# Optimization experiments

Hardware: AMD Instinct MI355X
Metric: run time of the kernel (lower is better)

Reference implementation:

```python
import jax, jax.numpy as jnp
import numpy as np
from jax.scipy.stats import norm

K = 2               # select_experts
NOISE_EPS = 0.01
LOSS_COEF = 0.01
CV_EPS = 1e-10


def setup_inputs() -> dict:
    key = jax.random.key(0)
    ks = jax.random.split(key, 8)
    N, D, H, E = 8192, 1024, 4096, 8
    s_in = 1.0 / np.sqrt(D)
    s_h = 1.0 / np.sqrt(H)
    return {
        "x": jax.random.normal(ks[0], (N, D), jnp.float32),
        "noise": jax.random.normal(ks[1], (N, E), jnp.float32),
        "w_gate": jax.random.normal(ks[2], (D, E), jnp.float32) * s_in,
        "w_noise": jax.random.normal(ks[3], (D, E), jnp.float32) * s_in,
        "W1": jax.random.normal(ks[4], (E, D, H), jnp.float32) * s_in,
        "b1": jnp.zeros((E, H), jnp.float32),
        "W2": jax.random.normal(ks[5], (E, H, D), jnp.float32) * s_h,
        "b2": jnp.zeros((E, D), jnp.float32),
    }


def _cv_squared(v):
    # torch .var() is unbiased (ddof=1)
    return v.var(ddof=1) / (v.mean() ** 2 + CV_EPS)


def reference(x, noise, w_gate, w_noise, W1, b1, W2, b2):
    N = x.shape[0]
    # --- noisy top-k gating (training path) ---
    clean_logits = x @ w_gate                                  # [N, E]
    noise_stddev = jax.nn.softplus(x @ w_noise) + NOISE_EPS    # [N, E]
    noisy_logits = clean_logits + noise * noise_stddev         # [N, E]
    top_vals, top_idx = jax.lax.top_k(noisy_logits, K + 1)     # [N, K+1]
    top_k_gates = jax.nn.softmax(top_vals[:, :K], axis=1)      # [N, K]
    gates = jnp.zeros_like(noisy_logits).at[
        jnp.arange(N)[:, None], top_idx[:, :K]
    ].set(top_k_gates)                                         # [N, E]

    # --- load (prob of being in top-k under the gating noise) ---
    thr_in = top_vals[:, K:K + 1]                              # [N, 1]
    thr_out = top_vals[:, K - 1:K]                             # [N, 1]
    is_in = noisy_logits > thr_in
    prob_in = norm.cdf((clean_logits - thr_in) / noise_stddev)
    prob_out = norm.cdf((clean_logits - thr_out) / noise_stddev)
    load = jnp.where(is_in, prob_in, prob_out).sum(0)          # [E]

    importance = gates.sum(0)                                  # [E]
    loss = (_cv_squared(importance) + _cv_squared(load)) * LOSS_COEF

    # --- dense all-expert stack, masked by sparse gates ---
    h = jax.nn.relu(jnp.einsum('nd,edh->neh', x, W1) + b1)     # [N, E, H]
    out = jnp.einsum('neh,ehd->ned', h, W2) + b2               # [N, E, D]
    y = jnp.einsum('ned,ne->nd', out, gates)                   # [N, D]
    return y, loss
```

## Files before the change

### kernel.cpp

```cpp
#include <hip/hip_runtime.h>

typedef unsigned short u16;
typedef unsigned int u32;
typedef __attribute__((ext_vector_type(4))) float f32x4;
typedef __attribute__((ext_vector_type(8))) short short8;
typedef __attribute__((ext_vector_type(4))) unsigned short u16x4;

#define BARR __builtin_amdgcn_s_barrier()
#define VM4  asm volatile("s_waitcnt vmcnt(4)" ::: "memory")
#define VM0  asm volatile("s_waitcnt vmcnt(0)" ::: "memory")

__device__ __forceinline__ u16 f2b(float f){
  u32 u = __float_as_uint(f);
  u = (u + 0x7FFFu + ((u >> 16) & 1u)) >> 16;
  return (u16)u;
}
__device__ __forceinline__ float b2f(u16 h){ return __uint_as_float(((u32)h) << 16); }

__device__ __forceinline__ void gload16(const void* g, void* l){
  __builtin_amdgcn_global_load_lds((__attribute__((address_space(1))) void*)(g),
                                   (__attribute__((address_space(3))) void*)(l), 16, 0, 0);
}

__global__ __launch_bounds__(256) void transpose_cvt_kernel(const float* __restrict__ src,
                                                            u16* __restrict__ dst,
                                                            int R, int C){
  __shared__ float t[64][65];
  int e = blockIdx.z;
  size_t eo = (size_t)R * C * e;
  int c0 = blockIdx.x * 64, r0 = blockIdx.y * 64;
  int tid = threadIdx.x;
  int lr = tid >> 4, lc4 = (tid & 15) * 4;
  #pragma unroll
  for (int i = 0; i < 4; i++){
    int r = lr + i * 16;
    float4 v = *(const float4*)&src[eo + (size_t)(r0 + r) * C + c0 + lc4];
    t[r][lc4] = v.x; t[r][lc4 + 1] = v.y; t[r][lc4 + 2] = v.z; t[r][lc4 + 3] = v.w;
  }
  __syncthreads();
  #pragma unroll
  for (int i = 0; i < 4; i++){
    int c = lr + i * 16;
    u16x4 o = { f2b(t[lc4][c]), f2b(t[lc4 + 1][c]), f2b(t[lc4 + 2][c]), f2b(t[lc4 + 3][c]) };
    *(u16x4*)&dst[eo + (size_t)(c0 + c) * R + r0 + lc4] = o;
  }
}

__global__ __launch_bounds__(256) void gating_kernel(const float* __restrict__ x,
                                                     const float* __restrict__ nz,
                                                     const float* __restrict__ wg,
                                                     const float* __restrict__ wn,
                                                     int* __restrict__ counts,
                                                     int4* __restrict__ rowinfo,
                                                     float* __restrict__ loadrow,
                                                     u16* __restrict__ xb){
  __shared__ float wpart[16][4][17];
  int tid = threadIdx.x, w = tid >> 6, lane = tid & 63;
  int d0 = w * 256 + lane * 4;
  float4 wgA[4], wgB[4], wnA[4], wnB[4];
  #pragma unroll
  for (int k = 0; k < 4; k++){
    wgA[k] = *(const float4*)&wg[(d0 + k) * 8];
    wgB[k] = *(const float4*)&wg[(d0 + k) * 8 + 4];
    wnA[k] = *(const float4*)&wn[(d0 + k) * 8];
    wnB[k] = *(const float4*)&wn[(d0 + k) * 8 + 4];
  }
  int rbase = blockIdx.x * 16;
  for (int r = 0; r < 16; r++){
    int row = rbase + r;
    float4 xv = *(const float4*)&x[(size_t)row * 1024 + d0];
    u16x4 xo = { f2b(xv.x), f2b(xv.y), f2b(xv.z), f2b(xv.w) };
    *(u16x4*)&xb[(size_t)row * 1024 + d0] = xo;
    float ag[8], an[8];
    #pragma unroll
    for (int e = 0; e < 8; e++){ ag[e] = 0.f; an[e] = 0.f; }
    float xk[4] = { xv.x, xv.y, xv.z, xv.w };
    #pragma unroll
    for (int k = 0; k < 4; k++){
      ag[0] = fmaf(xk[k], wgA[k].x, ag[0]); ag[1] = fmaf(xk[k], wgA[k].y, ag[1]);
      ag[2] = fmaf(xk[k], wgA[k].z, ag[2]); ag[3] = fmaf(xk[k], wgA[k].w, ag[3]);
      ag[4] = fmaf(xk[k], wgB[k].x, ag[4]); ag[5] = fmaf(xk[k], wgB[k].y, ag[5]);
      ag[6] = fmaf(xk[k], wgB[k].z, ag[6]); ag[7] = fmaf(xk[k], wgB[k].w, ag[7]);
      an[0] = fmaf(xk[k], wnA[k].x, an[0]); an[1] = fmaf(xk[k], wnA[k].y, an[1]);
      an[2] = fmaf(xk[k], wnA[k].z, an[2]); an[3] = fmaf(xk[k], wnA[k].w, an[3]);
      an[4] = fmaf(xk[k], wnB[k].x, an[4]); an[5] = fmaf(xk[k], wnB[k].y, an[5]);
      an[6] = fmaf(xk[k], wnB[k].z, an[6]); an[7] = fmaf(xk[k], wnB[k].w, an[7]);
    }
    #pragma unroll
    for (int off = 32; off >= 1; off >>= 1){
      #pragma unroll
      for (int e = 0; e < 8; e++){
        ag[e] += __shfl_xor(ag[e], off, 64);
        an[e] += __shfl_xor(an[e], off, 64);
      }
    }
    if (lane == 0){
      #pragma unroll
      for (int e = 0; e < 8; e++){
        wpart[r][w][e] = ag[e];
        wpart[r][w][8 + e] = an[e];
      }
    }
  }
  __syncthreads();
  if (tid < 16){
    int r = tid, row = rbase + r;
    float cg[16];
    #pragma unroll
    for (int v = 0; v < 16; v++)
      cg[v] = wpart[r][0][v] + wpart[r][1][v] + wpart[r][2][v] + wpart[r][3][v];
    float clean[8], sd[8], noisy[8];
    #pragma unroll
    for (int e = 0; e < 8; e++){
      clean[e] = cg[e];
      float v = cg[8 + e];
      float sp = fmaxf(v, 0.f) + log1pf(expf(-fabsf(v)));
      sd[e] = sp + 0.01f;
      noisy[e] = clean[e] + nz[row * 8 + e] * sd[e];
    }
    int i0 = 0, i1 = -1;
    float b0 = -3.4e38f, b1v = -3.4e38f, b2v = -3.4e38f;
    #pragma unroll
    for (int j = 0; j < 8; j++){
      float t = noisy[j];
      if (t > b0){ b2v = b1v; b1v = b0; i1 = i0; b0 = t; i0 = j; }
      else if (t > b1v){ b2v = b1v; b1v = t; i1 = j; }
      else if (t > b2v){ b2v = t; }
    }
    float eg = expf(b1v - b0);
    float g0 = 1.f / (1.f + eg), g1 = eg / (1.f + eg);
    rowinfo[row] = make_int4(i0, i1, __float_as_int(g0), __float_as_int(g1));
    atomicAdd(&counts[i0], 1);
    atomicAdd(&counts[i1], 1);
    float thr_in = b2v, thr_out = b1v;
    #pragma unroll
    for (int e = 0; e < 8; e++){
      bool isin = noisy[e] > thr_in;
      float thr = isin ? thr_in : thr_out;
      float z = (clean[e] - thr) / sd[e];
      loadrow[row * 8 + e] = 0.5f * (1.f + erff(z * 0.70710678118654752f));
    }
  }
}

__global__ void scan_kernel(const int* __restrict__ counts, int* __restrict__ offs,
                            int* __restrict__ btab){
  if (threadIdx.x == 0){
    int s = 0, nb = 0;
    for (int e = 0; e < 8; e++){
      offs[e] = s;
      int c = counts[e]; s += c;
      int nbe = (c + 255) >> 8;
      for (int t = 0; t < nbe; t++) btab[nb++] = (e << 16) | t;
    }
    offs[15] = nb;
  }
}

__global__ __launch_bounds__(256) void fill_kernel(const int4* __restrict__ rowinfo,
                                                   const int* __restrict__ offs,
                                                   int* __restrict__ cnt2,
                                                   int* __restrict__ tok,
                                                   int* __restrict__ slot_of){
  int r = blockIdx.x * 256 + threadIdx.x;
  int4 ri = rowinfo[r];
  int p0 = atomicAdd(&cnt2[ri.x], 1);
  int s0 = offs[ri.x] + p0;
  tok[s0] = r; slot_of[2 * r] = s0;
  int p1 = atomicAdd(&cnt2[ri.y], 1);
  int s1 = offs[ri.y] + p1;
  tok[s1] = r; slot_of[2 * r + 1] = s1;
}

template<int KDIM, bool GATHER, bool RELU, bool PSPLIT>
__global__ __launch_bounds__(512, 1) void ffn8_kernel(
    const u16* __restrict__ Ag, const u16* __restrict__ Bt,
    const float* __restrict__ bias, u16* __restrict__ outp,
    const int* __restrict__ counts, const int* __restrict__ offs,
    const int* __restrict__ btab, const int* __restrict__ tok,
    int nc, int klen, int ostr, size_t pstride)
{
  __shared__ u16 As[2][2][128 * 64];
  __shared__ u16 Bs[2][2][128 * 64];

  int gx = gridDim.x;
  int lin = blockIdx.y * gx + blockIdx.x;
  int total = gx * gridDim.y, chunk = total >> 3;
  int swz = (lin & 7) * chunk + (lin >> 3);
  int bx = swz % gx, tq = swz / gx;
  int nblk = offs[15];
  if (bx >= nblk) return;
  int kh = tq / nc;
  int tn = tq - kh * nc;
  int kbase = kh * klen;
  int niter = klen >> 7;
  int et = btab[bx]; int e = et >> 16, tm = et & 0xffff;
  int cnt = counts[e], off_e = offs[e];

  int tid = threadIdx.x, lane = tid & 63;
  int wid = tid >> 6, wm = wid >> 2, wn = wid & 3;

  int rl0 = tid >> 3, c8 = tid & 7;
  const char* Abase = (const char*)Ag + (size_t)kbase * 2;
  const char* Bbase = (const char*)(Bt + (size_t)e * 4194304) + (size_t)kbase * 2;
  u32 aoff[4], boff[4];
  #pragma unroll
  for (int h = 0; h < 2; h++)
    #pragma unroll
    for (int r = 0; r < 2; r++){
      int rl = h * 128 + r * 64 + rl0;
      int c8s = c8 ^ (rl & 7);
      int rr = tm * 256 + rl;
      int rc = (rr < cnt) ? rr : (cnt - 1);
      size_t arow = GATHER ? (size_t)tok[off_e + rc] : (size_t)(off_e + rc);
      aoff[h * 2 + r] = (u32)(arow * (KDIM * 2) + c8s * 16);
      boff[h * 2 + r] = (u32)((size_t)(tn * 256 + rl) * (KDIM * 2) + c8s * 16);
    }
  int ldst = (tid & ~63) * 8;

  auto stA = [&](int b, int h, int t){
    const char* s = Abase + (size_t)t * 128;
    gload16(s + aoff[h * 2 + 0], &As[b][h][ldst]);
    gload16(s + aoff[h * 2 + 1], &As[b][h][4096 + ldst]);
  };
  auto stB = [&](int b, int h, int t){
    const char* s = Bbase + (size_t)t * 128;
    gload16(s + boff[h * 2 + 0], &Bs[b][h][ldst]);
    gload16(s + boff[h * 2 + 1], &Bs[b][h][4096 + ldst]);
  };

  int lm = lane & 15, lkb = (lane >> 4) * 8;
  short8 Ar[4][2], Br[2][2][2];
  auto ldA = [&](int b, int rh){
    #pragma unroll
    for (int ii = 0; ii < 4; ii++){
      int rl = rh * 64 + ii * 16 + lm;
      #pragma unroll
      for (int ks = 0; ks < 2; ks++){
        int idx = (rl * 64 + ks * 32 + lkb) ^ ((rl & 7) << 3);
        Ar[ii][ks] = *(const short8*)&As[b][wm][idx];
      }
    }
  };
  auto ldB = [&](int b, int ch){
    #pragma unroll
    for (int jj = 0; jj < 2; jj++){
      int rb = wn * 64 + ch * 32 + jj * 16 + lm;
      int hB = rb >> 7, rl = rb & 127;
      #pragma unroll
      for (int ks = 0; ks < 2; ks++){
        int idx = (rl * 64 + ks * 32 + lkb) ^ ((rl & 7) << 3);
        Br[ch][jj][ks] = *(const short8*)&Bs[b][hB][idx];
      }
    }
  };

  f32x4 acc[8][4];
  #pragma unroll
  for (int i = 0; i < 8; i++)
    #pragma unroll
    for (int j = 0; j < 4; j++) acc[i][j] = (f32x4){0.f, 0.f, 0.f, 0.f};

  auto mfmaQ = [&](int rh, int ch){
    __builtin_amdgcn_s_setprio(1);
    #pragma unroll
    for (int ks = 0; ks < 2; ks++)
      #pragma unroll
      for (int ii = 0; ii < 4; ii++)
        #pragma unroll
        for (int jj = 0; jj < 2; jj++)
          acc[rh * 4 + ii][ch * 2 + jj] = __builtin_amdgcn_mfma_f32_16x16x32_bf16(
              Ar[ii][ks], Br[ch][jj][ks], acc[rh * 4 + ii][ch * 2 + jj], 0, 0, 0);
    __builtin_amdgcn_s_setprio(0);
  };

  stA(0, 0, 0); stA(0, 1, 0); stB(0, 0, 0); stB(0, 1, 0);
  stB(1, 0, 1); stA(1, 0, 1);
  VM4; BARR;

  for (int j = 0; j < niter - 1; ++j){
    int t1 = 2 * j + 1, t2 = 2 * j + 2, t3 = 2 * j + 3;
    ldA(0, 0); ldB(0, 0);
    stA(1, 1, t1);
    BARR; mfmaQ(0, 0); ldB(0, 1); BARR;
    stB(1, 1, t1);
    BARR; mfmaQ(0, 1); ldA(0, 1); BARR;
    stB(0, 0, t2);
    BARR; mfmaQ(1, 1); BARR;
    stA(0, 0, t2);
    BARR; mfmaQ(1, 0); VM4; BARR;
    ldA(1, 0); ldB(1, 0);
    stA(0, 1, t2);
    BARR; mfmaQ(0, 0); ldB(1, 1); BARR;
    stB(0, 1, t2);
    BARR; mfmaQ(0, 1); ldA(1, 1); BARR;
    stB(1, 0, t3);
    BARR; mfmaQ(1, 1); BARR;
    stA(1, 0, t3);
    BARR; mfmaQ(1, 0); VM4; BARR;
  }

  {
    int t1 = (klen >> 6) - 1;
    ldA(0, 0); ldB(0, 0);
    stA(1, 1, t1);
    BARR; mfmaQ(0, 0); ldB(0, 1); BARR;
    stB(1, 1, t1);
    BARR; mfmaQ(0, 1); ldA(0, 1); BARR;
    BARR; mfmaQ(1, 1); BARR;
    mfmaQ(1, 0); VM0; BARR;
    ldA(1, 0); ldB(1, 0);
    BARR; mfmaQ(0, 0); ldB(1, 1); BARR;
    BARR; mfmaQ(0, 1); ldA(1, 1); BARR;
    BARR; mfmaQ(1, 1); BARR;
    mfmaQ(1, 0);
  }

  int lr = (lane >> 4) * 4;
  u16* po = outp + (PSPLIT ? (size_t)kh * pstride : 0);
  #pragma unroll
  for (int i = 0; i < 8; i++){
    int row_l = wm * 128 + i * 16 + lr;
    #pragma unroll
    for (int jj = 0; jj < 4; jj++){
      int col = tn * 256 + wn * 64 + jj * 16 + lm;
      float bv = PSPLIT ? 0.f : bias[e * ostr + col];
      #pragma unroll
      for (int q = 0; q < 4; q++){
        int r = tm * 256 + row_l + q;
        if (r < cnt){
          float v = acc[i][jj][q] + bv;
          if (RELU) v = fmaxf(v, 0.f);
          po[(size_t)(off_e + r) * ostr + col] = f2b(v);
        }
      }
    }
  }
}

__global__ __launch_bounds__(256) void combine_kernel(const u16* __restrict__ pb,
                                                      const float* __restrict__ b2,
                                                      const int4* __restrict__ rowinfo,
                                                      const int* __restrict__ slot_of,
                                                      float* __restrict__ y){
  const size_t PS = (size_t)16384 * 1024;
  int g = blockIdx.x * 256 + threadIdx.x;
  int row = g >> 8;
  int c4 = (g & 255) * 4;
  int4 ri = rowinfo[row];
  float g0 = __int_as_float(ri.z), g1 = __int_as_float(ri.w);
  int s0 = slot_of[2 * row], s1 = slot_of[2 * row + 1];
  float4 sum0 = *(const float4*)&b2[(ri.x << 10) + c4];
  float4 sum1 = *(const float4*)&b2[(ri.y << 10) + c4];
  #pragma unroll
  for (int kh = 0; kh < 4; kh++){
    u16x4 a = *(const u16x4*)&pb[kh * PS + ((size_t)s0 << 10) + c4];
    u16x4 b = *(const u16x4*)&pb[kh * PS + ((size_t)s1 << 10) + c4];
    sum0.x += b2f(a.x); sum0.y += b2f(a.y); sum0.z += b2f(a.z); sum0.w += b2f(a.w);
    sum1.x += b2f(b.x); sum1.y += b2f(b.y); sum1.z += b2f(b.z); sum1.w += b2f(b.w);
  }
  float4 o;
  o.x = g0 * sum0.x + g1 * sum1.x;
  o.y = g0 * sum0.y + g1 * sum1.y;
  o.z = g0 * sum0.z + g1 * sum1.z;
  o.w = g0 * sum0.w + g1 * sum1.w;
  *(float4*)&y[(size_t)row * 1024 + c4] = o;
}

__global__ __launch_bounds__(256) void loss1_kernel(const int4* __restrict__ rowinfo,
                                                    const float* __restrict__ loadrow,
                                                    float* __restrict__ partials){
  __shared__ float part[16][256];
  int tid = threadIdx.x;
  int r = blockIdx.x * 256 + tid;
  int4 ri = rowinfo[r];
  float g0 = __int_as_float(ri.z), g1 = __int_as_float(ri.w);
  f32x4 l0 = *(const f32x4*)&loadrow[r * 8];
  f32x4 l1 = *(const f32x4*)&loadrow[r * 8 + 4];
  #pragma unroll
  for (int e = 0; e < 8; e++){
    part[e][tid] = ((ri.x == e) ? g0 : 0.f) + ((ri.y == e) ? g1 : 0.f);
    part[8 + e][tid] = (e < 4) ? l0[e & 3] : l1[e & 3];
  }
  __syncthreads();
  #pragma unroll
  for (int s = 128; s >= 1; s >>= 1){
    if (tid < s){
      #pragma unroll
      for (int e = 0; e < 16; e++) part[e][tid] += part[e][tid + s];
    }
    __syncthreads();
  }
  if (tid < 16) partials[blockIdx.x * 16 + tid] = part[tid][0];
}

__global__ __launch_bounds__(64) void loss2_kernel(const float* __restrict__ partials,
                                                   float* __restrict__ out_loss){
  __shared__ float tot[16];
  int tid = threadIdx.x;
  if (tid < 16){
    float s = 0.f;
    for (int b = 0; b < 32; b++) s += partials[b * 16 + tid];
    tot[tid] = s;
  }
  __syncthreads();
  if (tid == 0){
    float mi = 0.f, ml = 0.f;
    for (int e = 0; e < 8; e++){ mi += tot[e]; ml += tot[8 + e]; }
    mi *= 0.125f; ml *= 0.125f;
    float vi = 0.f, vl = 0.f;
    for (int e = 0; e < 8; e++){
      float di = tot[e] - mi; vi += di * di;
      float dl = tot[8 + e] - ml; vl += dl * dl;
    }
    vi /= 7.f; vl /= 7.f;
    float cvi = vi / (mi * mi + 1e-10f);
    float cvl = vl / (ml * ml + 1e-10f);
    out_loss[0] = 0.01f * (cvi + cvl);
  }
}

extern "C" void kernel_launch(void* const* d_in, const int* in_sizes, int n_in,
                              void* d_out, int out_size, void* d_ws, size_t ws_size,
                              hipStream_t stream){
  const float* x  = (const float*)d_in[0];
  const float* nz = (const float*)d_in[1];
  const float* wg = (const float*)d_in[2];
  const float* wn = (const float*)d_in[3];
  const float* W1 = (const float*)d_in[4];
  const float* b1 = (const float*)d_in[5];
  const float* W2 = (const float*)d_in[6];
  const float* b2 = (const float*)d_in[7];
  float* y = (float*)d_out;
  float* loss = y + (size_t)8192 * 1024;

  char* ws = (char*)d_ws;
  size_t o = 0;
  auto alloc = [&](size_t bytes){ size_t r = o; o += (bytes + 255) & ~(size_t)255; return r; };
  int*  counts  = (int*)(ws + alloc(64));
  int*  cnt2    = (int*)(ws + alloc(64));
  int*  offs    = (int*)(ws + alloc(64));
  int*  btab    = (int*)(ws + alloc(1024));
  int4* rowinfo = (int4*)(ws + alloc((size_t)8192 * 16));
  int*  slot_of = (int*)(ws + alloc((size_t)16384 * 4));
  int*  tok     = (int*)(ws + alloc((size_t)16384 * 4));
  float* loadrow = (float*)(ws + alloc((size_t)8192 * 8 * 4));
  float* partials = (float*)(ws + alloc(32 * 16 * 4));
  u16*  xb      = (u16*)(ws + alloc((size_t)8192 * 1024 * 2));
  u16*  w1t     = (u16*)(ws + alloc((size_t)8 * 1024 * 4096 * 2));
  u16*  w2t     = (u16*)(ws + alloc((size_t)8 * 1024 * 4096 * 2));
  u16*  h_buf   = (u16*)(ws + alloc((size_t)16384 * 4096 * 2));
  u16*  pbuf    = (u16*)(ws + alloc((size_t)4 * 16384 * 1024 * 2));
  if (o > ws_size) return;

  hipMemsetAsync(ws, 0, 768, stream);

  gating_kernel<<<512, 256, 0, stream>>>(x, nz, wg, wn, counts, rowinfo, loadrow, xb);
  transpose_cvt_kernel<<<dim3(64, 16, 8), 256, 0, stream>>>(W1, w1t, 1024, 4096);
  transpose_cvt_kernel<<<dim3(16, 64, 8), 256, 0, stream>>>(W2, w2t, 4096, 1024);
  scan_kernel<<<1, 64, 0, stream>>>(counts, offs, btab);
  fill_kernel<<<32, 256, 0, stream>>>(rowinfo, offs, cnt2, tok, slot_of);
  ffn8_kernel<1024, true, true, false><<<dim3(72, 16), 512, 0, stream>>>(
      xb, w1t, b1, h_buf, counts, offs, btab, tok, 16, 1024, 4096, 0);
  ffn8_kernel<4096, false, false, true><<<dim3(72, 16), 512, 0, stream>>>(
      h_buf, w2t, nullptr, pbuf, counts, offs, btab, tok, 4, 1024, 1024,
      (size_t)16384 * 1024);
  combine_kernel<<<8192, 256, 0, stream>>>(pbuf, b2, rowinfo, slot_of, y);
  loss1_kernel<<<32, 256, 0, stream>>>(rowinfo, loadrow, partials);
  loss2_kernel<<<1, 64, 0, stream>>>(partials, loss);
}
```

Before: 685.4 us.

## Stage GEMM epilogue through LDS for coalesced stores, merge scan into fill

Result: slower. 710.0 us (+3.6%).

```diff
diff --git a/kernel.cpp b/kernel.cpp
--- a/kernel.cpp
+++ b/kernel.cpp
@@ -143,32 +143,35 @@
   }
 }
 
-__global__ void scan_kernel(const int* __restrict__ counts, int* __restrict__ offs,
-                            int* __restrict__ btab){
-  if (threadIdx.x == 0){
-    int s = 0, nb = 0;
-    for (int e = 0; e < 8; e++){
-      offs[e] = s;
-      int c = counts[e]; s += c;
-      int nbe = (c + 255) >> 8;
-      for (int t = 0; t < nbe; t++) btab[nb++] = (e << 16) | t;
-    }
-    offs[15] = nb;
-  }
-}
-
-__global__ __launch_bounds__(256) void fill_kernel(const int4* __restrict__ rowinfo,
-                                                   const int* __restrict__ offs,
+__global__ __launch_bounds__(256) void fill_kernel(const int* __restrict__ counts,
+                                                   const int4* __restrict__ rowinfo,
+                                                   int* __restrict__ offs,
                                                    int* __restrict__ cnt2,
                                                    int* __restrict__ tok,
-                                                   int* __restrict__ slot_of){
+                                                   int* __restrict__ slot_of,
+                                                   int* __restrict__ btab){
+  __shared__ int loff[8];
+  if (threadIdx.x == 0){
+    int s = 0;
+    for (int e = 0; e < 8; e++){ loff[e] = s; s += counts[e]; }
+    if (blockIdx.x == 0){
+      int nb = 0;
+      for (int e = 0; e < 8; e++){
+        offs[e] = loff[e];
+        int nbe = (counts[e] + 255) >> 8;
+        for (int t = 0; t < nbe; t++) btab[nb++] = (e << 16) | t;
+      }
+      offs[15] = nb;
+    }
+  }
+  __syncthreads();
   int r = blockIdx.x * 256 + threadIdx.x;
   int4 ri = rowinfo[r];
   int p0 = atomicAdd(&cnt2[ri.x], 1);
-  int s0 = offs[ri.x] + p0;
+  int s0 = loff[ri.x] + p0;
   tok[s0] = r; slot_of[2 * r] = s0;
   int p1 = atomicAdd(&cnt2[ri.y], 1);
-  int s1 = offs[ri.y] + p1;
+  int s1 = loff[ri.y] + p1;
   tok[s1] = r; slot_of[2 * r + 1] = s1;
 }
 
@@ -180,8 +183,9 @@
     const int* __restrict__ btab, const int* __restrict__ tok,
     int nc, int klen, int ostr, size_t pstride)
 {
-  __shared__ u16 As[2][2][128 * 64];
-  __shared__ u16 Bs[2][2][128 * 64];
+  __shared__ u16 SMEM[65536];
+  u16 (*As)[2][8192] = (u16(*)[2][8192])SMEM;
+  u16 (*Bs)[2][8192] = (u16(*)[2][8192])(SMEM + 32768);
 
   int gx = gridDim.x;
   int lin = blockIdx.y * gx + blockIdx.x;
@@ -316,24 +320,37 @@
     mfmaQ(1, 0);
   }
 
-  int lr = (lane >> 4) * 4;
+  BARR;
   u16* po = outp + (PSPLIT ? (size_t)kh * pstride : 0);
+  int lr4 = (lane >> 4) * 4;
   #pragma unroll
   for (int i = 0; i < 8; i++){
-    int row_l = wm * 128 + i * 16 + lr;
+    int rl = wm * 128 + i * 16 + lr4;
     #pragma unroll
     for (int jj = 0; jj < 4; jj++){
-      int col = tn * 256 + wn * 64 + jj * 16 + lm;
-      float bv = PSPLIT ? 0.f : bias[e * ostr + col];
+      int col = wn * 64 + jj * 16 + lm;
+      float bv = PSPLIT ? 0.f : bias[e * ostr + tn * 256 + col];
       #pragma unroll
       for (int q = 0; q < 4; q++){
-        int r = tm * 256 + row_l + q;
-        if (r < cnt){
-          float v = acc[i][jj][q] + bv;
-          if (RELU) v = fmaxf(v, 0.f);
-          po[(size_t)(off_e + r) * ostr + col] = f2b(v);
-        }
-      }
+        int row = rl + q;
+        float v = acc[i][jj][q] + bv;
+        if (RELU) v = fmaxf(v, 0.f);
+        int g = (col >> 3) ^ (row & 7);
+        SMEM[row * 256 + (g << 3) + (col & 7)] = f2b(v);
+      }
+    }
+  }
+  BARR;
+  int srow = tid >> 5;
+  int scg  = tid & 31;
+  #pragma unroll
+  for (int p = 0; p < 16; p++){
+    int row = p * 16 + srow;
+    int g = scg ^ (row & 7);
+    short8 vv = *(const short8*)&SMEM[row * 256 + (g << 3)];
+    int grow = tm * 256 + row;
+    if (grow < cnt){
+      *(short8*)(po + (size_t)(off_e + grow) * ostr + tn * 256 + (scg << 3)) = vv;
     }
   }
 }
@@ -344,27 +361,32 @@
                                                       const int* __restrict__ slot_of,
                                                       float* __restrict__ y){
   const size_t PS = (size_t)16384 * 1024;
-  int g = blockIdx.x * 256 + threadIdx.x;
-  int row = g >> 8;
-  int c4 = (g & 255) * 4;
+  int w = threadIdx.x >> 6, lane = threadIdx.x & 63;
+  int row = blockIdx.x * 4 + w;
   int4 ri = rowinfo[row];
   float g0 = __int_as_float(ri.z), g1 = __int_as_float(ri.w);
   int s0 = slot_of[2 * row], s1 = slot_of[2 * row + 1];
-  float4 sum0 = *(const float4*)&b2[(ri.x << 10) + c4];
-  float4 sum1 = *(const float4*)&b2[(ri.y << 10) + c4];
-  #pragma unroll
-  for (int kh = 0; kh < 4; kh++){
-    u16x4 a = *(const u16x4*)&pb[kh * PS + ((size_t)s0 << 10) + c4];
-    u16x4 b = *(const u16x4*)&pb[kh * PS + ((size_t)s1 << 10) + c4];
-    sum0.x += b2f(a.x); sum0.y += b2f(a.y); sum0.z += b2f(a.z); sum0.w += b2f(a.w);
-    sum1.x += b2f(b.x); sum1.y += b2f(b.y); sum1.z += b2f(b.z); sum1.w += b2f(b.w);
-  }
-  float4 o;
-  o.x = g0 * sum0.x + g1 * sum1.x;
-  o.y = g0 * sum0.y + g1 * sum1.y;
-  o.z = g0 * sum0.z + g1 * sum1.z;
-  o.w = g0 * sum0.w + g1 * sum1.w;
-  *(float4*)&y[(size_t)row * 1024 + c4] = o;
+  const u16* pa = pb + ((size_t)s0 << 10);
+  const u16* pbb = pb + ((size_t)s1 << 10);
+  #pragma unroll
+  for (int k = 0; k < 4; k++){
+    int c4 = k * 256 + lane * 4;
+    float4 sum0 = *(const float4*)&b2[(ri.x << 10) + c4];
+    float4 sum1 = *(const float4*)&b2[(ri.y << 10) + c4];
+    #pragma unroll
+    for (int kh = 0; kh < 4; kh++){
+      u16x4 a = *(const u16x4*)&pa[kh * PS + c4];
+      u16x4 b = *(const u16x4*)&pbb[kh * PS + c4];
+      sum0.x += b2f(a.x); sum0.y += b2f(a.y); sum0.z += b2f(a.z); sum0.w += b2f(a.w);
+      sum1.x += b2f(b.x); sum1.y += b2f(b.y); sum1.z += b2f(b.z); sum1.w += b2f(b.w);
+    }
+    float4 o;
+    o.x = g0 * sum0.x + g1 * sum1.x;
+    o.y = g0 * sum0.y + g1 * sum1.y;
+    o.z = g0 * sum0.z + g1 * sum1.z;
+    o.w = g0 * sum0.w + g1 * sum1.w;
+    *(float4*)&y[(size_t)row * 1024 + c4] = o;
+  }
 }
 
 __global__ __launch_bounds__(256) void loss1_kernel(const int4* __restrict__ rowinfo,
@@ -458,14 +480,13 @@
   gating_kernel<<<512, 256, 0, stream>>>(x, nz, wg, wn, counts, rowinfo, loadrow, xb);
   transpose_cvt_kernel<<<dim3(64, 16, 8), 256, 0, stream>>>(W1, w1t, 1024, 4096);
   transpose_cvt_kernel<<<dim3(16, 64, 8), 256, 0, stream>>>(W2, w2t, 4096, 1024);
-  scan_kernel<<<1, 64, 0, stream>>>(counts, offs, btab);
-  fill_kernel<<<32, 256, 0, stream>>>(rowinfo, offs, cnt2, tok, slot_of);
+  fill_kernel<<<32, 256, 0, stream>>>(counts, rowinfo, offs, cnt2, tok, slot_of, btab);
   ffn8_kernel<1024, true, true, false><<<dim3(72, 16), 512, 0, stream>>>(
       xb, w1t, b1, h_buf, counts, offs, btab, tok, 16, 1024, 4096, 0);
   ffn8_kernel<4096, false, false, true><<<dim3(72, 16), 512, 0, stream>>>(
       h_buf, w2t, nullptr, pbuf, counts, offs, btab, tok, 4, 1024, 1024,
       (size_t)16384 * 1024);
-  combine_kernel<<<8192, 256, 0, stream>>>(pbuf, b2, rowinfo, slot_of, y);
+  combine_kernel<<<2048, 256, 0, stream>>>(pbuf, b2, rowinfo, slot_of, y);
   loss1_kernel<<<32, 256, 0, stream>>>(rowinfo, loadrow, partials);
   loss2_kernel<<<1, 64, 0, stream>>>(partials, loss);
 }
```
